# Optimization experiments

Measured on AMD Instinct MI355X. Metric: run time of the kernel, lower is better.

Reference implementation:

```python
import math
import jax, jax.numpy as jnp
import numpy as np

DIM, WIN, HEADS, NW, B = 256, 64, 8, 256, 8
B_ = NW * B  # 2048 windowed batches


def _nest_idcs(window_size):
    # Morton / Z-order (HEALPix nested) index for each pixel of an s x s window
    s = int(round(math.sqrt(window_size)))
    bits = int(round(math.log2(s)))
    idx = np.zeros((s, s), np.int64)
    for i in range(s):
        for j in range(s):
            m = 0
            for b in range(bits):
                m |= ((i >> b) & 1) << (2 * b + 1)
                m |= ((j >> b) & 1) << (2 * b)
            idx[i, j] = m
    return idx


def _rel_pos_index(window_size):
    s = int(round(math.sqrt(window_size)))
    coords = np.stack(np.meshgrid(np.arange(s), np.arange(s), indexing='ij'))  # (2,s,s)
    cf = coords.reshape(2, -1)
    rel = cf[:, :, None] - cf[:, None, :]          # (2,N,N)
    rel = rel.transpose(1, 2, 0).copy()            # (N,N,2)
    rel[:, :, 0] += s - 1
    rel[:, :, 1] += s - 1
    rel[:, :, 0] *= 2 * s - 1
    rpi = rel.sum(-1)                              # (N,N)
    inv = _nest_idcs(window_size).flatten().argsort()
    rpi = rpi[inv][:, inv]                         # reorder into nested pixel order
    return rpi.astype(np.int32)


def setup_inputs() -> dict:
    key = jax.random.key(0)
    ks = jax.random.split(key, 6)
    x = jax.random.normal(ks[0], (B_, WIN, DIM), dtype=jnp.float32)
    # shifted-window style 0 / -100 additive mask
    mask = jnp.where(jax.random.uniform(ks[1], (NW, WIN, WIN)) < 0.9, 0.0, -100.0).astype(jnp.float32)
    qkv_w = jax.random.normal(ks[2], (3 * DIM, DIM), dtype=jnp.float32) * (DIM ** -0.5)
    qkv_b = jnp.zeros((3 * DIM,), jnp.float32)
    proj_w = jax.random.normal(ks[3], (DIM, DIM), dtype=jnp.float32) * (DIM ** -0.5)
    proj_b = jnp.zeros((DIM,), jnp.float32)
    logit_scale = jnp.log(10.0 * jnp.ones((HEADS, 1, 1), jnp.float32))
    s = int(round(math.sqrt(WIN)))
    rel_bias_table = 0.02 * jax.random.normal(ks[4], ((2 * s - 1) ** 2, HEADS), dtype=jnp.float32)
    rel_pos_index = jnp.asarray(_rel_pos_index(WIN))
    return {"x": x, "mask": mask, "qkv_w": qkv_w, "qkv_b": qkv_b, "proj_w": proj_w,
            "proj_b": proj_b, "logit_scale": logit_scale, "rel_bias_table": rel_bias_table,
            "rel_pos_index": rel_pos_index}


def reference(x, mask, qkv_w, qkv_b, proj_w, proj_b, logit_scale, rel_bias_table, rel_pos_index):
    Bw, N, C = x.shape
    H = logit_scale.shape[0]
    hd = C // H
    qkv = (x @ qkv_w.T + qkv_b).reshape(Bw, N, 3, H, hd).transpose(2, 0, 3, 1, 4)
    q, k, v = qkv[0], qkv[1], qkv[2]  # each (Bw, H, N, hd)
    # cosine attention (Swin v2): L2-normalize q, k; learnable clamped logit scale
    qn = q / jnp.maximum(jnp.linalg.norm(q, axis=-1, keepdims=True), 1e-12)
    kn = k / jnp.maximum(jnp.linalg.norm(k, axis=-1, keepdims=True), 1e-12)
    attn = jnp.einsum('bhnd,bhmd->bhnm', qn, kn)
    ls = jnp.exp(jnp.minimum(logit_scale, jnp.log(jnp.asarray(100.0, x.dtype))))
    attn = attn * ls  # (H,1,1) broadcasts over (Bw,H,N,N)
    # relative position bias gather: (N,N,H) -> (H,N,N)
    bias = rel_bias_table[rel_pos_index].transpose(2, 0, 1)
    attn = attn + bias[None]
    # shifted-window mask add
    nW = mask.shape[0]
    attn = attn.reshape(Bw // nW, nW, H, N, N) + mask[None, :, None]
    attn = jax.nn.softmax(attn.reshape(Bw, H, N, N), axis=-1)
    out = jnp.einsum('bhnm,bhmd->bhnd', attn, v).transpose(0, 2, 1, 3).reshape(Bw, N, C)
    return out @ proj_w.T + proj_b
```

## Files before the change

kernel.cpp:

```cpp
#include <hip/hip_runtime.h>

typedef unsigned short u16;
typedef u16   u16x4 __attribute__((ext_vector_type(4)));
typedef u16   u16x8 __attribute__((ext_vector_type(8)));
typedef short s16x4 __attribute__((ext_vector_type(4)));
typedef __bf16 bf16x8 __attribute__((ext_vector_type(8)));
typedef float f32x4 __attribute__((ext_vector_type(4)));

#define LDP 264
#define VTP 72

__device__ __forceinline__ u16 f2b(float f) {
  union { float f; unsigned u; } c; c.f = f;
  return (u16)((c.u + 0x7fffu + ((c.u >> 16) & 1u)) >> 16);
}
__device__ __forceinline__ float b2f(u16 h) {
  union { unsigned u; float f; } c; c.u = ((unsigned)h) << 16;
  return c.f;
}
__device__ __forceinline__ bf16x8 ld16(const u16* p) {
  return __builtin_bit_cast(bf16x8, *reinterpret_cast<const u16x8*>(p));
}
__device__ __forceinline__ f32x4 z4() { f32x4 z; z[0]=0.f; z[1]=0.f; z[2]=0.f; z[3]=0.f; return z; }

__global__ void prep_kernel(const float* __restrict__ qkv_w, const float* __restrict__ proj_w,
                            const float* __restrict__ mask, const float* __restrict__ table,
                            const int* __restrict__ rpi,
                            u16* __restrict__ wq, u16* __restrict__ wp,
                            float* __restrict__ biasT, float* __restrict__ maskT) {
  int i = blockIdx.x * 512 + threadIdx.x;
  if (i < 196608) { wq[i] = f2b(qkv_w[i]); return; }
  i -= 196608;
  if (i < 65536) { wp[i] = f2b(proj_w[i]); return; }
  i -= 65536;
  if (i < 32768) {
    int h = i >> 12, a = (i >> 6) & 63, q = i & 63;
    biasT[i] = table[rpi[q * 64 + a] * 8 + h];
    return;
  }
  i -= 32768;
  if (i < 1048576) {
    int w = i >> 12, a = (i >> 6) & 63, q = i & 63;
    maskT[i] = mask[(w << 12) + (q << 6) + a];
  }
}

__global__ __launch_bounds__(512, 2) void winattn_kernel(
    const float* __restrict__ x, const float* __restrict__ qkv_b,
    const float* __restrict__ proj_b, const float* __restrict__ logit_scale,
    const u16* __restrict__ wq, const u16* __restrict__ wp,
    const float* __restrict__ biasT, const float* __restrict__ maskT,
    float* __restrict__ out) {
  __shared__ u16 qL[64][LDP];
  __shared__ u16 kL[64][LDP];
  __shared__ u16 vT[256][VTP];
  __shared__ u16 xb[64][LDP];

  const int b    = blockIdx.x;
  const int tid  = threadIdx.x;
  const int wave = tid >> 6;
  const int lane = tid & 63;
  const int lr   = lane & 15;
  const int lg   = lane >> 4;

  const float4* xg4 = reinterpret_cast<const float4*>(x + (size_t)b * 16384);
#pragma unroll
  for (int j = 0; j < 8; ++j) {
    int e4 = tid + j * 512;
    float4 v = xg4[e4];
    int e = e4 * 4, tok = e >> 8, c = e & 255;
    u16x4 h;
    h[0] = f2b(v.x); h[1] = f2b(v.y); h[2] = f2b(v.z); h[3] = f2b(v.w);
    *reinterpret_cast<u16x4*>(&xb[tok][c]) = h;
  }
  __syncthreads();

#pragma unroll 1
  for (int ng = 0; ng < 2; ++ng) {
    const int nb0 = wave * 96 + ng * 48;
    const u16* wrow0 = wq + (nb0 +  0 + lr) * 256 + lg * 8;
    const u16* wrow1 = wq + (nb0 + 16 + lr) * 256 + lg * 8;
    const u16* wrow2 = wq + (nb0 + 32 + lr) * 256 + lg * 8;
    f32x4 acc[3][4];
#pragma unroll
    for (int j = 0; j < 3; ++j)
#pragma unroll
      for (int mt = 0; mt < 4; ++mt) acc[j][mt] = z4();
#pragma unroll
    for (int ks = 0; ks < 8; ++ks) {
      bf16x8 bf0 = ld16(wrow0 + ks * 32);
      bf16x8 bf1 = ld16(wrow1 + ks * 32);
      bf16x8 bf2 = ld16(wrow2 + ks * 32);
#pragma unroll
      for (int mt = 0; mt < 4; ++mt) {
        bf16x8 af = ld16(&xb[mt * 16 + lr][ks * 32 + lg * 8]);
        acc[0][mt] = __builtin_amdgcn_mfma_f32_16x16x32_bf16(af, bf0, acc[0][mt], 0, 0, 0);
        acc[1][mt] = __builtin_amdgcn_mfma_f32_16x16x32_bf16(af, bf1, acc[1][mt], 0, 0, 0);
        acc[2][mt] = __builtin_amdgcn_mfma_f32_16x16x32_bf16(af, bf2, acc[2][mt], 0, 0, 0);
      }
    }
#pragma unroll
    for (int j = 0; j < 3; ++j) {
      const int nb = nb0 + j * 16;
      const int colg = nb + lr;
      const float bias = qkv_b[colg];
      const int seg = nb >> 8;
#pragma unroll
      for (int mt = 0; mt < 4; ++mt) {
#pragma unroll
        for (int r = 0; r < 4; ++r) {
          int row = mt * 16 + lg * 4 + r;
          u16 hv = f2b(acc[j][mt][r] + bias);
          if (seg == 0)      qL[row][colg] = hv;
          else if (seg == 1) kL[row][colg - 256] = hv;
          else               vT[colg - 512][row] = hv;
        }
      }
    }
  }
  __syncthreads();

#pragma unroll
  for (int t2 = 0; t2 < 2; ++t2) {
    int task = tid + t2 * 512;
    int qk  = task >> 9;
    int tok = (task >> 3) & 63;
    int h   = task & 7;
    u16* base = qk ? &kL[tok][h * 32] : &qL[tok][h * 32];
    float v[32];
    float ss = 0.f;
#pragma unroll
    for (int j4 = 0; j4 < 4; ++j4) {
      u16x8 u = *reinterpret_cast<u16x8*>(base + j4 * 8);
#pragma unroll
      for (int j = 0; j < 8; ++j) { float f = b2f(u[j]); v[j4 * 8 + j] = f; ss += f * f; }
    }
    float inv = 1.0f / fmaxf(sqrtf(ss), 1e-12f);
    if (!qk) inv *= __expf(fminf(logit_scale[h], 4.6051702f));
#pragma unroll
    for (int j4 = 0; j4 < 4; ++j4) {
      u16x8 u;
#pragma unroll
      for (int j = 0; j < 8; ++j) u[j] = f2b(v[j4 * 8 + j] * inv);
      *reinterpret_cast<u16x8*>(base + j4 * 8) = u;
    }
  }
  __syncthreads();

  {
    const int h = wave;
    bf16x8 kf[4], qf[4];
#pragma unroll
    for (int t = 0; t < 4; ++t) {
      kf[t] = ld16(&kL[t * 16 + lr][h * 32 + lg * 8]);
      qf[t] = ld16(&qL[t * 16 + lr][h * 32 + lg * 8]);
    }
    f32x4 st[4][4];
#pragma unroll
    for (int kt = 0; kt < 4; ++kt)
#pragma unroll
      for (int qt = 0; qt < 4; ++qt)
        st[kt][qt] = __builtin_amdgcn_mfma_f32_16x16x32_bf16(kf[kt], qf[qt], z4(), 0, 0, 0);

    const float* bT = biasT + h * 4096;
    const float* mT = maskT + (size_t)(b & 255) * 4096;
#pragma unroll
    for (int kt = 0; kt < 4; ++kt)
#pragma unroll
      for (int qt = 0; qt < 4; ++qt)
#pragma unroll
        for (int r = 0; r < 4; ++r) {
          int ktok = kt * 16 + lg * 4 + r, qtok = qt * 16 + lr;
          st[kt][qt][r] += bT[ktok * 64 + qtok] + mT[ktok * 64 + qtok];
        }

#pragma unroll
    for (int qt = 0; qt < 4; ++qt) {
      float m = -1e30f;
#pragma unroll
      for (int kt = 0; kt < 4; ++kt)
#pragma unroll
        for (int r = 0; r < 4; ++r) m = fmaxf(m, st[kt][qt][r]);
      m = fmaxf(m, __shfl_xor(m, 16));
      m = fmaxf(m, __shfl_xor(m, 32));
      float s = 0.f;
#pragma unroll
      for (int kt = 0; kt < 4; ++kt)
#pragma unroll
        for (int r = 0; r < 4; ++r) {
          float e = __expf(st[kt][qt][r] - m);
          st[kt][qt][r] = e; s += e;
        }
      s += __shfl_xor(s, 16);
      s += __shfl_xor(s, 32);
      float inv = 1.0f / s;
#pragma unroll
      for (int kt = 0; kt < 4; ++kt)
#pragma unroll
        for (int r = 0; r < 4; ++r) st[kt][qt][r] *= inv;
    }

    f32x4 o[4][2];
#pragma unroll
    for (int qt = 0; qt < 4; ++qt)
#pragma unroll
      for (int dt = 0; dt < 2; ++dt) o[qt][dt] = z4();
#pragma unroll
    for (int kt = 0; kt < 4; ++kt) {
      s16x4 pa[4];
#pragma unroll
      for (int qt = 0; qt < 4; ++qt)
#pragma unroll
        for (int i = 0; i < 4; ++i) pa[qt][i] = (short)f2b(st[kt][qt][i]);
#pragma unroll
      for (int dt = 0; dt < 2; ++dt) {
        s16x4 vf = *reinterpret_cast<const s16x4*>(&vT[h * 32 + dt * 16 + lr][kt * 16 + lg * 4]);
#pragma unroll
        for (int qt = 0; qt < 4; ++qt)
          o[qt][dt] = __builtin_amdgcn_mfma_f32_16x16x16bf16_1k(pa[qt], vf, o[qt][dt], 0, 0, 0);
      }
    }
#pragma unroll
    for (int qt = 0; qt < 4; ++qt)
#pragma unroll
      for (int dt = 0; dt < 2; ++dt)
#pragma unroll
        for (int r = 0; r < 4; ++r) {
          int qtok = qt * 16 + lg * 4 + r;
          xb[qtok][h * 32 + dt * 16 + lr] = f2b(o[qt][dt][r]);
        }
  }
  __syncthreads();

  {
    const int nb0 = wave * 32;
    const u16* wrow0 = wp + (nb0 +  0 + lr) * 256 + lg * 8;
    const u16* wrow1 = wp + (nb0 + 16 + lr) * 256 + lg * 8;
    f32x4 acc[2][4];
#pragma unroll
    for (int j = 0; j < 2; ++j)
#pragma unroll
      for (int mt = 0; mt < 4; ++mt) acc[j][mt] = z4();
#pragma unroll
    for (int ks = 0; ks < 8; ++ks) {
      bf16x8 bf0 = ld16(wrow0 + ks * 32);
      bf16x8 bf1 = ld16(wrow1 + ks * 32);
#pragma unroll
      for (int mt = 0; mt < 4; ++mt) {
        bf16x8 af = ld16(&xb[mt * 16 + lr][ks * 32 + lg * 8]);
        acc[0][mt] = __builtin_amdgcn_mfma_f32_16x16x32_bf16(af, bf0, acc[0][mt], 0, 0, 0);
        acc[1][mt] = __builtin_amdgcn_mfma_f32_16x16x32_bf16(af, bf1, acc[1][mt], 0, 0, 0);
      }
    }
    float* og = out + (size_t)b * 16384;
#pragma unroll
    for (int j = 0; j < 2; ++j) {
      const int colg = nb0 + j * 16 + lr;
      const float pbv = proj_b[colg];
#pragma unroll
      for (int mt = 0; mt < 4; ++mt)
#pragma unroll
        for (int r = 0; r < 4; ++r) {
          int row = mt * 16 + lg * 4 + r;
          og[row * 256 + colg] = acc[j][mt][r] + pbv;
        }
    }
  }
}

extern "C" void kernel_launch(void* const* d_in, const int* in_sizes, int n_in,
                              void* d_out, int out_size, void* d_ws, size_t ws_size,
                              hipStream_t stream) {
  const float* x    = (const float*)d_in[0];
  const float* mask = (const float*)d_in[1];
  const float* qw   = (const float*)d_in[2];
  const float* qb   = (const float*)d_in[3];
  const float* pw   = (const float*)d_in[4];
  const float* pb   = (const float*)d_in[5];
  const float* ls   = (const float*)d_in[6];
  const float* tab  = (const float*)d_in[7];
  const int*   rpi  = (const int*)d_in[8];

  char* ws = (char*)d_ws;
  u16*   wqb   = (u16*)ws;
  u16*   wpb   = (u16*)(ws + 393216);
  float* biasT = (float*)(ws + 524288);
  float* maskT = (float*)(ws + 655360);

  prep_kernel<<<2624, 512, 0, stream>>>(qw, pw, mask, tab, rpi, wqb, wpb, biasT, maskT);
  winattn_kernel<<<2048, 512, 0, stream>>>(x, qb, pb, ls, wqb, wpb, biasT, maskT,
                                           (float*)d_out);
}
```

Baseline: 453.3 us.

## Keep per-head Q/K in registers, fuse L2 norm, pre-permute bias/mask to MFMA layout

Each wave now computes the Q, K and V projection for its own head, transposed so the output fragments land directly in MFMA operand layout. Q and K are L2-normalized in registers with cross-lane shuffles and never touch LDS, which removes the qL/kL buffers, a normalization pass and one barrier. Bias and mask are pre-permuted in the prep kernel into per-lane fragment order so each accumulator reads one float4. The smaller LDS footprint lets launch bounds request 4 blocks per CU, at the risk of register spills and more MFMA operand reloads of the weights.

```diff
diff --git a/kernel.cpp b/kernel.cpp
--- a/kernel.cpp
+++ b/kernel.cpp
@@ -8,7 +8,7 @@
 typedef float f32x4 __attribute__((ext_vector_type(4)));
 
 #define LDP 264
-#define VTP 72
+#define VTP 68
 
 __device__ __forceinline__ u16 f2b(float f) {
   union { float f; unsigned u; } c; c.f = f;
@@ -27,38 +27,40 @@
                             const float* __restrict__ mask, const float* __restrict__ table,
                             const int* __restrict__ rpi,
                             u16* __restrict__ wq, u16* __restrict__ wp,
-                            float* __restrict__ biasT, float* __restrict__ maskT) {
+                            float* __restrict__ biasP, float* __restrict__ maskP) {
   int i = blockIdx.x * 512 + threadIdx.x;
   if (i < 196608) { wq[i] = f2b(qkv_w[i]); return; }
   i -= 196608;
   if (i < 65536) { wp[i] = f2b(proj_w[i]); return; }
   i -= 65536;
   if (i < 32768) {
-    int h = i >> 12, a = (i >> 6) & 63, q = i & 63;
-    biasT[i] = table[rpi[q * 64 + a] * 8 + h];
+    int r = i & 3, lane = (i >> 2) & 63, qt = (i >> 8) & 3, kt = (i >> 10) & 3, h = i >> 12;
+    int qtok = qt * 16 + (lane & 15);
+    int ktok = kt * 16 + (lane >> 4) * 4 + r;
+    biasP[i] = table[rpi[qtok * 64 + ktok] * 8 + h];
     return;
   }
   i -= 32768;
   if (i < 1048576) {
-    int w = i >> 12, a = (i >> 6) & 63, q = i & 63;
-    maskT[i] = mask[(w << 12) + (q << 6) + a];
-  }
-}
-
-__global__ __launch_bounds__(512, 2) void winattn_kernel(
+    int r = i & 3, lane = (i >> 2) & 63, qt = (i >> 8) & 3, kt = (i >> 10) & 3, w = i >> 12;
+    int qtok = qt * 16 + (lane & 15);
+    int ktok = kt * 16 + (lane >> 4) * 4 + r;
+    maskP[i] = mask[(w << 12) + qtok * 64 + ktok];
+  }
+}
+
+__global__ __launch_bounds__(512, 4) void winattn_kernel(
     const float* __restrict__ x, const float* __restrict__ qkv_b,
     const float* __restrict__ proj_b, const float* __restrict__ logit_scale,
     const u16* __restrict__ wq, const u16* __restrict__ wp,
-    const float* __restrict__ biasT, const float* __restrict__ maskT,
+    const float* __restrict__ biasP, const float* __restrict__ maskP,
     float* __restrict__ out) {
-  __shared__ u16 qL[64][LDP];
-  __shared__ u16 kL[64][LDP];
+  __shared__ u16 xb[64][LDP];
   __shared__ u16 vT[256][VTP];
-  __shared__ u16 xb[64][LDP];
 
   const int b    = blockIdx.x;
   const int tid  = threadIdx.x;
-  const int wave = tid >> 6;
+  const int h    = tid >> 6;
   const int lane = tid & 63;
   const int lr   = lane & 15;
   const int lg   = lane >> 4;
@@ -69,110 +71,132 @@
     int e4 = tid + j * 512;
     float4 v = xg4[e4];
     int e = e4 * 4, tok = e >> 8, c = e & 255;
-    u16x4 h;
-    h[0] = f2b(v.x); h[1] = f2b(v.y); h[2] = f2b(v.z); h[3] = f2b(v.w);
-    *reinterpret_cast<u16x4*>(&xb[tok][c]) = h;
+    u16x4 hv;
+    hv[0] = f2b(v.x); hv[1] = f2b(v.y); hv[2] = f2b(v.z); hv[3] = f2b(v.w);
+    *reinterpret_cast<u16x4*>(&xb[tok][c]) = hv;
   }
   __syncthreads();
 
-#pragma unroll 1
-  for (int ng = 0; ng < 2; ++ng) {
-    const int nb0 = wave * 96 + ng * 48;
-    const u16* wrow0 = wq + (nb0 +  0 + lr) * 256 + lg * 8;
-    const u16* wrow1 = wq + (nb0 + 16 + lr) * 256 + lg * 8;
-    const u16* wrow2 = wq + (nb0 + 32 + lr) * 256 + lg * 8;
-    f32x4 acc[3][4];
-#pragma unroll
-    for (int j = 0; j < 3; ++j)
-#pragma unroll
-      for (int mt = 0; mt < 4; ++mt) acc[j][mt] = z4();
+  s16x4 qf[2][4], kf[2][4];
+
+  {
+    f32x4 a0[4], a1[4];
+#pragma unroll
+    for (int tt = 0; tt < 4; ++tt) { a0[tt] = z4(); a1[tt] = z4(); }
+    const u16* w0 = wq + (h * 32 + lr) * 256 + lg * 8;
 #pragma unroll
     for (int ks = 0; ks < 8; ++ks) {
-      bf16x8 bf0 = ld16(wrow0 + ks * 32);
-      bf16x8 bf1 = ld16(wrow1 + ks * 32);
-      bf16x8 bf2 = ld16(wrow2 + ks * 32);
-#pragma unroll
-      for (int mt = 0; mt < 4; ++mt) {
-        bf16x8 af = ld16(&xb[mt * 16 + lr][ks * 32 + lg * 8]);
-        acc[0][mt] = __builtin_amdgcn_mfma_f32_16x16x32_bf16(af, bf0, acc[0][mt], 0, 0, 0);
-        acc[1][mt] = __builtin_amdgcn_mfma_f32_16x16x32_bf16(af, bf1, acc[1][mt], 0, 0, 0);
-        acc[2][mt] = __builtin_amdgcn_mfma_f32_16x16x32_bf16(af, bf2, acc[2][mt], 0, 0, 0);
-      }
-    }
-#pragma unroll
-    for (int j = 0; j < 3; ++j) {
-      const int nb = nb0 + j * 16;
-      const int colg = nb + lr;
-      const float bias = qkv_b[colg];
-      const int seg = nb >> 8;
-#pragma unroll
-      for (int mt = 0; mt < 4; ++mt) {
-#pragma unroll
-        for (int r = 0; r < 4; ++r) {
-          int row = mt * 16 + lg * 4 + r;
-          u16 hv = f2b(acc[j][mt][r] + bias);
-          if (seg == 0)      qL[row][colg] = hv;
-          else if (seg == 1) kL[row][colg - 256] = hv;
-          else               vT[colg - 512][row] = hv;
-        }
+      bf16x8 wf0 = ld16(w0 + ks * 32);
+      bf16x8 wf1 = ld16(w0 + 4096 + ks * 32);
+#pragma unroll
+      for (int tt = 0; tt < 4; ++tt) {
+        bf16x8 xf = ld16(&xb[tt * 16 + lr][ks * 32 + lg * 8]);
+        a0[tt] = __builtin_amdgcn_mfma_f32_16x16x32_bf16(wf0, xf, a0[tt], 0, 0, 0);
+        a1[tt] = __builtin_amdgcn_mfma_f32_16x16x32_bf16(wf1, xf, a1[tt], 0, 0, 0);
+      }
+    }
+    f32x4 bb0 = *reinterpret_cast<const f32x4*>(qkv_b + h * 32 + lg * 4);
+    f32x4 bb1 = *reinterpret_cast<const f32x4*>(qkv_b + h * 32 + 16 + lg * 4);
+    float lsv = __expf(fminf(logit_scale[h], 4.6051702f));
+#pragma unroll
+    for (int tt = 0; tt < 4; ++tt) {
+      a0[tt] += bb0; a1[tt] += bb1;
+      float ss = 0.f;
+#pragma unroll
+      for (int r = 0; r < 4; ++r) ss += a0[tt][r] * a0[tt][r] + a1[tt][r] * a1[tt][r];
+      ss += __shfl_xor(ss, 16);
+      ss += __shfl_xor(ss, 32);
+      float inv = lsv / fmaxf(sqrtf(ss), 1e-12f);
+#pragma unroll
+      for (int r = 0; r < 4; ++r) {
+        qf[0][tt][r] = (short)f2b(a0[tt][r] * inv);
+        qf[1][tt][r] = (short)f2b(a1[tt][r] * inv);
+      }
+    }
+  }
+  {
+    f32x4 a0[4], a1[4];
+#pragma unroll
+    for (int tt = 0; tt < 4; ++tt) { a0[tt] = z4(); a1[tt] = z4(); }
+    const u16* w0 = wq + (256 + h * 32 + lr) * 256 + lg * 8;
+#pragma unroll
+    for (int ks = 0; ks < 8; ++ks) {
+      bf16x8 wf0 = ld16(w0 + ks * 32);
+      bf16x8 wf1 = ld16(w0 + 4096 + ks * 32);
+#pragma unroll
+      for (int tt = 0; tt < 4; ++tt) {
+        bf16x8 xf = ld16(&xb[tt * 16 + lr][ks * 32 + lg * 8]);
+        a0[tt] = __builtin_amdgcn_mfma_f32_16x16x32_bf16(wf0, xf, a0[tt], 0, 0, 0);
+        a1[tt] = __builtin_amdgcn_mfma_f32_16x16x32_bf16(wf1, xf, a1[tt], 0, 0, 0);
+      }
+    }
+    f32x4 bb0 = *reinterpret_cast<const f32x4*>(qkv_b + 256 + h * 32 + lg * 4);
+    f32x4 bb1 = *reinterpret_cast<const f32x4*>(qkv_b + 256 + h * 32 + 16 + lg * 4);
+#pragma unroll
+    for (int tt = 0; tt < 4; ++tt) {
+      a0[tt] += bb0; a1[tt] += bb1;
+      float ss = 0.f;
+#pragma unroll
+      for (int r = 0; r < 4; ++r) ss += a0[tt][r] * a0[tt][r] + a1[tt][r] * a1[tt][r];
+      ss += __shfl_xor(ss, 16);
+      ss += __shfl_xor(ss, 32);
+      float inv = 1.0f / fmaxf(sqrtf(ss), 1e-12f);
+#pragma unroll
+      for (int r = 0; r < 4; ++r) {
+        kf[0][tt][r] = (short)f2b(a0[tt][r] * inv);
+        kf[1][tt][r] = (short)f2b(a1[tt][r] * inv);
+      }
+    }
+  }
+  {
+    f32x4 a0[4], a1[4];
+#pragma unroll
+    for (int tt = 0; tt < 4; ++tt) { a0[tt] = z4(); a1[tt] = z4(); }
+    const u16* w0 = wq + (512 + h * 32 + lr) * 256 + lg * 8;
+#pragma unroll
+    for (int ks = 0; ks < 8; ++ks) {
+      bf16x8 wf0 = ld16(w0 + ks * 32);
+      bf16x8 wf1 = ld16(w0 + 4096 + ks * 32);
+#pragma unroll
+      for (int tt = 0; tt < 4; ++tt) {
+        bf16x8 xf = ld16(&xb[tt * 16 + lr][ks * 32 + lg * 8]);
+        a0[tt] = __builtin_amdgcn_mfma_f32_16x16x32_bf16(wf0, xf, a0[tt], 0, 0, 0);
+        a1[tt] = __builtin_amdgcn_mfma_f32_16x16x32_bf16(wf1, xf, a1[tt], 0, 0, 0);
+      }
+    }
+    f32x4 bb0 = *reinterpret_cast<const f32x4*>(qkv_b + 512 + h * 32 + lg * 4);
+    f32x4 bb1 = *reinterpret_cast<const f32x4*>(qkv_b + 512 + h * 32 + 16 + lg * 4);
+#pragma unroll
+    for (int tt = 0; tt < 4; ++tt) {
+      a0[tt] += bb0; a1[tt] += bb1;
+#pragma unroll
+      for (int r = 0; r < 4; ++r) {
+        vT[h * 32 + lg * 4 + r][tt * 16 + lr] = f2b(a0[tt][r]);
+        vT[h * 32 + 16 + lg * 4 + r][tt * 16 + lr] = f2b(a1[tt][r]);
       }
     }
   }
   __syncthreads();
 
-#pragma unroll
-  for (int t2 = 0; t2 < 2; ++t2) {
-    int task = tid + t2 * 512;
-    int qk  = task >> 9;
-    int tok = (task >> 3) & 63;
-    int h   = task & 7;
-    u16* base = qk ? &kL[tok][h * 32] : &qL[tok][h * 32];
-    float v[32];
-    float ss = 0.f;
-#pragma unroll
-    for (int j4 = 0; j4 < 4; ++j4) {
-      u16x8 u = *reinterpret_cast<u16x8*>(base + j4 * 8);
-#pragma unroll
-      for (int j = 0; j < 8; ++j) { float f = b2f(u[j]); v[j4 * 8 + j] = f; ss += f * f; }
-    }
-    float inv = 1.0f / fmaxf(sqrtf(ss), 1e-12f);
-    if (!qk) inv *= __expf(fminf(logit_scale[h], 4.6051702f));
-#pragma unroll
-    for (int j4 = 0; j4 < 4; ++j4) {
-      u16x8 u;
-#pragma unroll
-      for (int j = 0; j < 8; ++j) u[j] = f2b(v[j4 * 8 + j] * inv);
-      *reinterpret_cast<u16x8*>(base + j4 * 8) = u;
-    }
-  }
-  __syncthreads();
-
-  {
-    const int h = wave;
-    bf16x8 kf[4], qf[4];
-#pragma unroll
-    for (int t = 0; t < 4; ++t) {
-      kf[t] = ld16(&kL[t * 16 + lr][h * 32 + lg * 8]);
-      qf[t] = ld16(&qL[t * 16 + lr][h * 32 + lg * 8]);
-    }
+  {
     f32x4 st[4][4];
 #pragma unroll
     for (int kt = 0; kt < 4; ++kt)
 #pragma unroll
-      for (int qt = 0; qt < 4; ++qt)
-        st[kt][qt] = __builtin_amdgcn_mfma_f32_16x16x32_bf16(kf[kt], qf[qt], z4(), 0, 0, 0);
-
-    const float* bT = biasT + h * 4096;
-    const float* mT = maskT + (size_t)(b & 255) * 4096;
+      for (int qt = 0; qt < 4; ++qt) {
+        f32x4 s = __builtin_amdgcn_mfma_f32_16x16x16bf16_1k(kf[0][kt], qf[0][qt], z4(), 0, 0, 0);
+        st[kt][qt] = __builtin_amdgcn_mfma_f32_16x16x16bf16_1k(kf[1][kt], qf[1][qt], s, 0, 0, 0);
+      }
+
+    const f32x4* bP = reinterpret_cast<const f32x4*>(biasP) + (size_t)h * 1024 + lane;
+    const f32x4* mP = reinterpret_cast<const f32x4*>(maskP) + (size_t)(b & 255) * 1024 + lane;
 #pragma unroll
     for (int kt = 0; kt < 4; ++kt)
 #pragma unroll
-      for (int qt = 0; qt < 4; ++qt)
-#pragma unroll
-        for (int r = 0; r < 4; ++r) {
-          int ktok = kt * 16 + lg * 4 + r, qtok = qt * 16 + lr;
-          st[kt][qt][r] += bT[ktok * 64 + qtok] + mT[ktok * 64 + qtok];
-        }
+      for (int qt = 0; qt < 4; ++qt) {
+        f32x4 ad = bP[(kt * 4 + qt) * 64] + mP[(kt * 4 + qt) * 64];
+        st[kt][qt] += ad;
+      }
 
 #pragma unroll
     for (int qt = 0; qt < 4; ++qt) {
@@ -233,9 +257,9 @@
   __syncthreads();
 
   {
-    const int nb0 = wave * 32;
-    const u16* wrow0 = wp + (nb0 +  0 + lr) * 256 + lg * 8;
-    const u16* wrow1 = wp + (nb0 + 16 + lr) * 256 + lg * 8;
+    const int nb0 = h * 32;
+    const u16* wrow0 = wp + (nb0 + lr) * 256 + lg * 8;
+    const u16* wrow1 = wrow0 + 4096;
     f32x4 acc[2][4];
 #pragma unroll
     for (int j = 0; j < 2; ++j)
@@ -284,10 +308,10 @@
   char* ws = (char*)d_ws;
   u16*   wqb   = (u16*)ws;
   u16*   wpb   = (u16*)(ws + 393216);
-  float* biasT = (float*)(ws + 524288);
-  float* maskT = (float*)(ws + 655360);
-
-  prep_kernel<<<2624, 512, 0, stream>>>(qw, pw, mask, tab, rpi, wqb, wpb, biasT, maskT);
-  winattn_kernel<<<2048, 512, 0, stream>>>(x, qb, pb, ls, wqb, wpb, biasT, maskT,
+  float* biasP = (float*)(ws + 524288);
+  float* maskP = (float*)(ws + 655360);
+
+  prep_kernel<<<2624, 512, 0, stream>>>(qw, pw, mask, tab, rpi, wqb, wpb, biasP, maskP);
+  winattn_kernel<<<2048, 512, 0, stream>>>(x, qb, pb, ls, wqb, wpb, biasP, maskP,
                                            (float*)d_out);
 }
```

Result: slower. 486.7 us (+7.4%).
